# Kernel optimization log

Measured on AMD Instinct MI355X. Metric: run time of the kernel, lower is better.

The kernel has to match this reference:

```python
import jax, jax.numpy as jnp
import numpy as np

B, S, E, D, OUT = 128, 128, 256, 256, 64


def setup_inputs() -> dict:
    key = jax.random.key(0)
    ks = jax.random.split(key, 10)
    w = lambda k, shp, s=0.05: (jax.random.normal(k, shp, dtype=jnp.float32) * s)
    return {
        "input_encoded": jax.random.normal(ks[0], (B, S, E), dtype=jnp.float32),
        "y_history": jax.random.normal(ks[1], (B, S, OUT), dtype=jnp.float32),
        "h0": jax.random.normal(ks[2], (B, D), dtype=jnp.float32) * 0.1,
        "c0": jax.random.normal(ks[3], (B, D), dtype=jnp.float32) * 0.1,
        "attn_W1": w(ks[4], (2 * D + E, E)),
        "attn_b1": jnp.zeros((E,), jnp.float32),
        "attn_w2": w(ks[5], (E,)),
        "attn_b2": jnp.zeros((1,), jnp.float32),
        "lstm_Wih": w(ks[6], (OUT, 4 * D)),
        "lstm_Whh": w(ks[7], (D, 4 * D)),
        "lstm_bih": jnp.zeros((4 * D,), jnp.float32),
        "lstm_bhh": jnp.zeros((4 * D,), jnp.float32),
        "fc_W": w(ks[8], (E + OUT, OUT)),
        "fc_b": jnp.zeros((OUT,), jnp.float32),
        "fc_out_W": w(ks[9], (D + E, OUT * S)),
        "fc_out_b": jnp.zeros((OUT * S,), jnp.float32),
    }


def reference(input_encoded, y_history, h0, c0, attn_W1, attn_b1, attn_w2, attn_b2,
              lstm_Wih, lstm_Whh, lstm_bih, lstm_bhh, fc_W, fc_b, fc_out_W, fc_out_b):
    # Split the attn first-layer weight according to the concat order (h, c, enc).
    Wh, Wc, We = attn_W1[:D], attn_W1[D:2 * D], attn_W1[2 * D:]
    # Encoder projection is time-invariant across decoder steps; hoist it.
    enc_proj = jnp.einsum('bse,ef->bsf', input_encoded, We)  # [B,S,E]

    def step(carry, y_t):
        h, c, _ = carry
        hc = h @ Wh + c @ Wc + attn_b1                       # [B,E]
        pre = jnp.tanh(enc_proj + hc[:, None, :])            # [B,S,E]
        scores = pre @ attn_w2 + attn_b2[0]                  # [B,S]
        alpha = jax.nn.softmax(scores, axis=1)
        context = jnp.einsum('bs,bse->be', alpha, input_encoded)  # [B,E]
        y_tilde = jnp.concatenate([context, y_t], axis=1) @ fc_W + fc_b  # [B,OUT]
        gates = y_tilde @ lstm_Wih + lstm_bih + h @ lstm_Whh + lstm_bhh  # [B,4D]
        i, f, g, o = jnp.split(gates, 4, axis=1)  # pytorch gate order i,f,g,o
        c_new = jax.nn.sigmoid(f) * c + jax.nn.sigmoid(i) * jnp.tanh(g)
        h_new = jax.nn.sigmoid(o) * jnp.tanh(c_new)
        return (h_new, c_new, context), None

    y_seq = jnp.transpose(y_history, (1, 0, 2))  # [S,B,OUT]
    (h_T, c_T, context_T), _ = jax.lax.scan(step, (h0, c0, jnp.zeros((B, E), h0.dtype)), y_seq)
    out = jnp.concatenate([h_T, context_T], axis=1) @ fc_out_W + fc_out_b  # [B,OUT*S]
    return out.reshape(-1, S, OUT)
```

## Files before the change

kernel.cpp:

```cpp
#include <hip/hip_runtime.h>

#define BB 128
#define SS 128
#define EE 256
#define DD 256
#define OO 64

#define W1_OFF   0
#define WHH_OFF  196608
#define WIH_OFF  458752
#define FCW_OFF  524288
#define WTOTAL   544768

__device__ __forceinline__ float fsig(float x) { return 1.0f / (1.0f + __expf(-x)); }
__device__ __forceinline__ float ftanh(float x) {
    float t = __expf(-2.0f * fabsf(x));
    float r = (1.0f - t) / (1.0f + t);
    return copysignf(r, x);
}
__device__ __forceinline__ int SWZ(int e) { return (e & ~31) | ((e + 4 * (e >> 5)) & 31); }

__device__ __forceinline__ void fma8(const uint4 w, const float xv, float* acc) {
    acc[0] += xv * __uint_as_float(w.x << 16);
    acc[1] += xv * __uint_as_float(w.x & 0xffff0000u);
    acc[2] += xv * __uint_as_float(w.y << 16);
    acc[3] += xv * __uint_as_float(w.y & 0xffff0000u);
    acc[4] += xv * __uint_as_float(w.z << 16);
    acc[5] += xv * __uint_as_float(w.z & 0xffff0000u);
    acc[6] += xv * __uint_as_float(w.w << 16);
    acc[7] += xv * __uint_as_float(w.w & 0xffff0000u);
}

__global__ __launch_bounds__(256) void conv_kernel(
    const float* __restrict__ W1, const float* __restrict__ Whh,
    const float* __restrict__ Wih, const float* __restrict__ fcW,
    unsigned short* __restrict__ out)
{
    const int idx = blockIdx.x * 256 + threadIdx.x;
    float f;
    if      (idx < WHH_OFF)  f = W1[idx];
    else if (idx < WIH_OFF)  f = Whh[idx - WHH_OFF];
    else if (idx < FCW_OFF)  f = Wih[idx - WIH_OFF];
    else if (idx < WTOTAL)   f = fcW[idx - FCW_OFF];
    else return;
    unsigned int u = __float_as_uint(f);
    u = (u + 0x7fffu + ((u >> 16) & 1u)) >> 16;
    out[idx] = (unsigned short)u;
}

__global__ __launch_bounds__(1024, 4) void scan_kernel(
    const float* __restrict__ inp,
    const float* __restrict__ yhist,
    const float* __restrict__ h0, const float* __restrict__ c0,
    const float* __restrict__ W1f,
    const float* __restrict__ b1, const float* __restrict__ w2, const float* __restrict__ b2,
    const float* __restrict__ bih, const float* __restrict__ bhh,
    const float* __restrict__ fcb,
    const unsigned short* __restrict__ wbf,
    float* __restrict__ hctxT)
{
    __shared__ float sh_h[DD], sh_c[DD], sh_hc[EE];
    __shared__ float sh_gh[1024];
    __shared__ float sh_w2[EE];
    __shared__ float sh_b1[EE], sh_bs[1024];
    __shared__ float sh_raw[SS];
    __shared__ float sh_ctx[EE], sh_y[OO], sh_yt[OO], sh_fcb[OO];
    __shared__ float sh_misc[1];
    __shared__ float red1[32 * 256];
    __shared__ float red2[8 * 1024];

    const int b = blockIdx.x, t = threadIdx.x;
    const float* inp_b = inp + b * SS * EE;
    const unsigned short* W1bf  = wbf + W1_OFF;
    const unsigned short* Whhbf = wbf + WHH_OFF;
    const unsigned short* Wihbf = wbf + WIH_OFF;
    const unsigned short* fcWbf = wbf + FCW_OFF;
    const float b2v = b2[0];

    const int e8  = (t & 31) * 8,  kc1 = t >> 5;
    const int j8  = (t & 127) * 8, kc2 = t >> 7;
    const int s_own = t >> 3,      a2  = t & 7, e0 = a2 * 32;
    const int e4  = (t & 63) * 4,  sc  = t >> 6;
    const int o4  = (t & 15) * 4,  kc3 = t >> 4;

    if (t < 256) {
        sh_h[t] = h0[b * 256 + t]; sh_c[t] = c0[b * 256 + t];
        sh_b1[t] = b1[t];
        sh_w2[SWZ(t)] = w2[t];
    }
    if (t < 64) sh_fcb[t] = fcb[t];
    sh_bs[t] = bih[t] + bhh[t];

    float er[32];
    #pragma unroll
    for (int j = 0; j < 32; ++j) er[j] = 0.f;
    {
        const float* We = W1f + 512 * 256;
        for (int kc = 0; kc < 16; ++kc) {
            {
                const int row = t >> 6, c4 = (t & 63) * 4;
                float4 v = *(const float4*)(We + (size_t)(kc * 16 + row) * 256 + c4);
                *(float4*)&red1[row * 256 + c4] = v;
            }
            {
                const int s = t >> 3, k2 = (t & 7) * 2;
                float2 v = *(const float2*)(inp_b + s * 256 + kc * 16 + k2);
                red1[4096 + s * 16 + k2] = v.x;
                red1[4096 + s * 16 + k2 + 1] = v.y;
            }
            __syncthreads();
            for (int k = 0; k < 16; ++k) {
                const float xv = red1[4096 + s_own * 16 + k];
                #pragma unroll
                for (int j4 = 0; j4 < 8; ++j4) {
                    float4 w = *(const float4*)&red1[k * 256 + e0 + j4 * 4];
                    er[j4*4+0] += xv * w.x; er[j4*4+1] += xv * w.y;
                    er[j4*4+2] += xv * w.z; er[j4*4+3] += xv * w.w;
                }
            }
            __syncthreads();
        }
    }

    for (int ts = 0; ts < SS; ++ts) {
        if (t < 64) sh_y[t] = yhist[b * SS * OO + ts * OO + t];

        {
            float acc[8];
            #pragma unroll
            for (int r = 0; r < 8; ++r) acc[r] = 0.f;
            #pragma unroll 4
            for (int k = kc1 * 16; k < kc1 * 16 + 16; ++k) {
                const float xv = (k < 256) ? sh_h[k] : sh_c[k - 256];
                uint4 w = *(const uint4*)(W1bf + (size_t)k * 256 + e8);
                fma8(w, xv, acc);
            }
            *(float4*)&red1[kc1 * 256 + e8]     = make_float4(acc[0], acc[1], acc[2], acc[3]);
            *(float4*)&red1[kc1 * 256 + e8 + 4] = make_float4(acc[4], acc[5], acc[6], acc[7]);
        }
        {
            float acc[8];
            #pragma unroll
            for (int r = 0; r < 8; ++r) acc[r] = 0.f;
            #pragma unroll 4
            for (int k = kc2 * 32; k < kc2 * 32 + 32; ++k) {
                const float hv = sh_h[k];
                uint4 w = *(const uint4*)(Whhbf + (size_t)k * 1024 + j8);
                fma8(w, hv, acc);
            }
            *(float4*)&red2[kc2 * 1024 + j8]     = make_float4(acc[0], acc[1], acc[2], acc[3]);
            *(float4*)&red2[kc2 * 1024 + j8 + 4] = make_float4(acc[4], acc[5], acc[6], acc[7]);
        }
        __syncthreads();
        if (t < 256) {
            float v = sh_b1[t];
            #pragma unroll 8
            for (int kc = 0; kc < 32; ++kc) v += red1[kc * 256 + t];
            sh_hc[SWZ(t)] = v;
        }
        {
            float v = 0.f;
            #pragma unroll
            for (int kc = 0; kc < 8; ++kc) v += red2[kc * 1024 + t];
            sh_gh[t] = v;
        }
        __syncthreads();

        {
            float acc = 0.f;
            #pragma unroll
            for (int j4 = 0; j4 < 8; ++j4) {
                const int phys = e0 + ((j4 * 4 + 4 * a2) & 31);
                float4 hc4 = *(const float4*)&sh_hc[phys];
                float4 w24 = *(const float4*)&sh_w2[phys];
                acc += ftanh(er[j4*4+0] + hc4.x) * w24.x;
                acc += ftanh(er[j4*4+1] + hc4.y) * w24.y;
                acc += ftanh(er[j4*4+2] + hc4.z) * w24.z;
                acc += ftanh(er[j4*4+3] + hc4.w) * w24.w;
            }
            acc += __shfl_xor(acc, 1);
            acc += __shfl_xor(acc, 2);
            acc += __shfl_xor(acc, 4);
            if (a2 == 0) sh_raw[s_own] = __expf(acc + b2v);
        }
        __syncthreads();
        if (t < 64) {
            float v = sh_raw[t] + sh_raw[t + 64];
            #pragma unroll
            for (int m = 32; m > 0; m >>= 1) v += __shfl_xor(v, m);
            if (t == 0) sh_misc[0] = 1.0f / v;
        }
        __syncthreads();

        {
            float ax = 0.f, ay = 0.f, az = 0.f, aw = 0.f;
            for (int s = sc * 8; s < sc * 8 + 8; ++s) {
                const float al = sh_raw[s];
                float4 iv = *(const float4*)(inp_b + s * 256 + e4);
                ax += al * iv.x; ay += al * iv.y; az += al * iv.z; aw += al * iv.w;
            }
            *(float4*)&red1[sc * 256 + e4] = make_float4(ax, ay, az, aw);
        }
        __syncthreads();
        if (t < 256) {
            float v = 0.f;
            #pragma unroll
            for (int k = 0; k < 16; ++k) v += red1[k * 256 + t];
            v *= sh_misc[0];
            sh_ctx[t] = v;
            if (ts == SS - 1) hctxT[(size_t)(256 + t) * 128 + b] = v;
        }
        __syncthreads();

        {
            float acc[4] = {0.f, 0.f, 0.f, 0.f};
            for (int kk = kc3 * 5; kk < kc3 * 5 + 5; ++kk) {
                const float val = (kk < 256) ? sh_ctx[kk] : sh_y[kk - 256];
                uint2 w = *(const uint2*)(fcWbf + kk * 64 + o4);
                acc[0] += val * __uint_as_float(w.x << 16);
                acc[1] += val * __uint_as_float(w.x & 0xffff0000u);
                acc[2] += val * __uint_as_float(w.y << 16);
                acc[3] += val * __uint_as_float(w.y & 0xffff0000u);
            }
            *(float4*)&red1[kc3 * 64 + o4] = make_float4(acc[0], acc[1], acc[2], acc[3]);
        }
        __syncthreads();
        if (t < 64) {
            float v = sh_fcb[t];
            #pragma unroll 16
            for (int kc = 0; kc < 64; ++kc) v += red1[kc * 64 + t];
            sh_yt[t] = v;
        }
        __syncthreads();

        {
            float acc[8];
            #pragma unroll
            for (int r = 0; r < 8; ++r) acc[r] = 0.f;
            #pragma unroll
            for (int k = kc2 * 8; k < kc2 * 8 + 8; ++k) {
                const float yv = sh_yt[k];
                uint4 w = *(const uint4*)(Wihbf + (size_t)k * 1024 + j8);
                fma8(w, yv, acc);
            }
            *(float4*)&red2[kc2 * 1024 + j8]     = make_float4(acc[0], acc[1], acc[2], acc[3]);
            *(float4*)&red2[kc2 * 1024 + j8 + 4] = make_float4(acc[4], acc[5], acc[6], acc[7]);
        }
        __syncthreads();
        {
            float v = sh_gh[t] + sh_bs[t];
            #pragma unroll
            for (int kc = 0; kc < 8; ++kc) v += red2[kc * 1024 + t];
            red1[t] = v;
        }
        __syncthreads();
        if (t < 256) {
            const float gi = red1[t], gf = red1[256 + t], gg = red1[512 + t], go = red1[768 + t];
            const float cn = fsig(gf) * sh_c[t] + fsig(gi) * ftanh(gg);
            sh_c[t] = cn;
            const float hn = fsig(go) * ftanh(cn);
            sh_h[t] = hn;
            if (ts == SS - 1) hctxT[(size_t)t * 128 + b] = hn;
        }
        __syncthreads();
    }
}

__global__ __launch_bounds__(256) void out_gemm(
    const float* __restrict__ AT, const float* __restrict__ W,
    const float* __restrict__ bias, float* __restrict__ out)
{
    __shared__ float Ab[64 * 132];
    __shared__ float Bb[64 * 32];
    const int t = threadIdx.x;
    const int nt = blockIdx.x * 32;
    const int n4 = (t & 7) * 4;
    const int m4 = (t >> 3) * 4;
    float acc[4][4];
    #pragma unroll
    for (int i = 0; i < 4; ++i)
        #pragma unroll
        for (int jj = 0; jj < 4; ++jj) acc[i][jj] = 0.f;

    for (int kc = 0; kc < 8; ++kc) {
        #pragma unroll
        for (int i = 0; i < 8; ++i) {
            const int flat4 = i * 256 + t;
            const int row = flat4 >> 5, mm4 = (flat4 & 31) * 4;
            float4 v = *(const float4*)(AT + (size_t)(kc * 64 + row) * 128 + mm4);
            *(float4*)&Ab[row * 132 + mm4] = v;
        }
        #pragma unroll
        for (int i = 0; i < 2; ++i) {
            const int fl = t + i * 256;
            const int k = fl >> 3, nn4 = (fl & 7) * 4;
            *(float4*)&Bb[k * 32 + nn4] =
                *(const float4*)(W + (size_t)(kc * 64 + k) * 8192 + nt + nn4);
        }
        __syncthreads();
        for (int k = 0; k < 64; ++k) {
            const float4 bv = *(const float4*)&Bb[k * 32 + n4];
            const float4 av = *(const float4*)&Ab[k * 132 + m4];
            acc[0][0] += av.x * bv.x; acc[0][1] += av.x * bv.y; acc[0][2] += av.x * bv.z; acc[0][3] += av.x * bv.w;
            acc[1][0] += av.y * bv.x; acc[1][1] += av.y * bv.y; acc[1][2] += av.y * bv.z; acc[1][3] += av.y * bv.w;
            acc[2][0] += av.z * bv.x; acc[2][1] += av.z * bv.y; acc[2][2] += av.z * bv.z; acc[2][3] += av.z * bv.w;
            acc[3][0] += av.w * bv.x; acc[3][1] += av.w * bv.y; acc[3][2] += av.w * bv.z; acc[3][3] += av.w * bv.w;
        }
        __syncthreads();
    }
    const float4 bb = *(const float4*)(bias + nt + n4);
    #pragma unroll
    for (int i = 0; i < 4; ++i) {
        float4 r;
        r.x = acc[i][0] + bb.x; r.y = acc[i][1] + bb.y;
        r.z = acc[i][2] + bb.z; r.w = acc[i][3] + bb.w;
        *(float4*)(out + (size_t)(m4 + i) * 8192 + nt + n4) = r;
    }
}

extern "C" void kernel_launch(void* const* d_in, const int* in_sizes, int n_in,
                              void* d_out, int out_size, void* d_ws, size_t ws_size,
                              hipStream_t stream) {
    const float* inp = (const float*)d_in[0];
    const float* yh  = (const float*)d_in[1];
    const float* h0  = (const float*)d_in[2];
    const float* c0  = (const float*)d_in[3];
    const float* W1  = (const float*)d_in[4];
    const float* b1  = (const float*)d_in[5];
    const float* w2  = (const float*)d_in[6];
    const float* b2  = (const float*)d_in[7];
    const float* Wih = (const float*)d_in[8];
    const float* Whh = (const float*)d_in[9];
    const float* bih = (const float*)d_in[10];
    const float* bhh = (const float*)d_in[11];
    const float* fcW = (const float*)d_in[12];
    const float* fcb = (const float*)d_in[13];
    const float* foW = (const float*)d_in[14];
    const float* fob = (const float*)d_in[15];

    float* hctxT = (float*)d_ws;
    unsigned short* wbf = (unsigned short*)d_out;

    conv_kernel<<<dim3((WTOTAL + 255) / 256), dim3(256), 0, stream>>>(W1, Whh, Wih, fcW, wbf);
    scan_kernel<<<dim3(BB), dim3(1024), 0, stream>>>(
        inp, yh, h0, c0, W1, b1, w2, b2, bih, bhh, fcb, wbf, hctxT);
    out_gemm<<<dim3(8192 / 32), dim3(256), 0, stream>>>(hctxT, foW, fob, (float*)d_out);
}
```

Measured before the change: 4.855 ms.

## Cache encoder input in LDS, prefetch Wih into registers, rebalance matvec splits

Loads the block's whole encoder input slice (128x256 floats, padded) into shared memory once, so the per-step context reduction reads LDS instead of global memory. It prefetches the Wih bf16 weights into registers ahead of the y_tilde dependency, so those global loads overlap the context and fc work. It also regroups the h/c and Whh matvecs into narrower columns with deeper k-chunks, separates the attention hc reduction so it finishes before the Whh matvec, and folds bias b1 into the encoder projection registers. The large shared buffer (about 150KB) raises LDS usage per block and adds register pressure from the prefetch array.

```diff
diff --git a/kernel.cpp b/kernel.cpp
--- a/kernel.cpp
+++ b/kernel.cpp
@@ -19,17 +19,8 @@
     return copysignf(r, x);
 }
 __device__ __forceinline__ int SWZ(int e) { return (e & ~31) | ((e + 4 * (e >> 5)) & 31); }
-
-__device__ __forceinline__ void fma8(const uint4 w, const float xv, float* acc) {
-    acc[0] += xv * __uint_as_float(w.x << 16);
-    acc[1] += xv * __uint_as_float(w.x & 0xffff0000u);
-    acc[2] += xv * __uint_as_float(w.y << 16);
-    acc[3] += xv * __uint_as_float(w.y & 0xffff0000u);
-    acc[4] += xv * __uint_as_float(w.z << 16);
-    acc[5] += xv * __uint_as_float(w.z & 0xffff0000u);
-    acc[6] += xv * __uint_as_float(w.w << 16);
-    acc[7] += xv * __uint_as_float(w.w & 0xffff0000u);
-}
+__device__ __forceinline__ float bflo(unsigned int u) { return __uint_as_float(u << 16); }
+__device__ __forceinline__ float bfhi(unsigned int u) { return __uint_as_float(u & 0xffff0000u); }
 
 __global__ __launch_bounds__(256) void conv_kernel(
     const float* __restrict__ W1, const float* __restrict__ Whh,
@@ -59,37 +50,44 @@
     const unsigned short* __restrict__ wbf,
     float* __restrict__ hctxT)
 {
-    __shared__ float sh_h[DD], sh_c[DD], sh_hc[EE];
-    __shared__ float sh_gh[1024];
+    __shared__ float sh_inp[SS * 260];
+    __shared__ float red[5 * 1024];
+    __shared__ float sh_h[DD], sh_c[DD];
+    __shared__ float sh_hc[EE];
     __shared__ float sh_w2[EE];
-    __shared__ float sh_b1[EE], sh_bs[1024];
     __shared__ float sh_raw[SS];
-    __shared__ float sh_ctx[EE], sh_y[OO], sh_yt[OO], sh_fcb[OO];
+    __shared__ float sh_ctx[EE];
+    __shared__ float sh_y[OO], sh_yt[OO];
     __shared__ float sh_misc[1];
-    __shared__ float red1[32 * 256];
-    __shared__ float red2[8 * 1024];
 
     const int b = blockIdx.x, t = threadIdx.x;
-    const float* inp_b = inp + b * SS * EE;
+    const float* inp_b = inp + (size_t)b * SS * EE;
     const unsigned short* W1bf  = wbf + W1_OFF;
     const unsigned short* Whhbf = wbf + WHH_OFF;
     const unsigned short* Wihbf = wbf + WIH_OFF;
     const unsigned short* fcWbf = wbf + FCW_OFF;
     const float b2v = b2[0];
 
-    const int e8  = (t & 31) * 8,  kc1 = t >> 5;
-    const int j8  = (t & 127) * 8, kc2 = t >> 7;
-    const int s_own = t >> 3,      a2  = t & 7, e0 = a2 * 32;
-    const int e4  = (t & 63) * 4,  sc  = t >> 6;
-    const int o4  = (t & 15) * 4,  kc3 = t >> 4;
-
+    const int c0_1 = (t & 63) * 4,  kg1 = t >> 6;
+    const int c0_2 = (t & 255) * 4, kg2 = t >> 8;
+    const int s_own = t >> 3, a2 = t & 7, e0 = a2 * 32;
+    const int c0_3 = (t & 127) * 2, sg3 = t >> 7;
+    const int o4 = (t & 15) * 4, kc3 = t >> 4;
+
+    const float bs_reg  = bih[t] + bhh[t];
+    const float fcb_reg = (t < 64) ? fcb[t] : 0.f;
+
+    #pragma unroll
+    for (int i = 0; i < 8; ++i) {
+        const int idx = i * 1024 + t;
+        const int s = idx >> 6, c4 = (idx & 63) * 4;
+        *(float4*)&sh_inp[s * 260 + c4] = *(const float4*)(inp_b + (size_t)idx * 4);
+    }
     if (t < 256) {
         sh_h[t] = h0[b * 256 + t]; sh_c[t] = c0[b * 256 + t];
-        sh_b1[t] = b1[t];
         sh_w2[SWZ(t)] = w2[t];
     }
-    if (t < 64) sh_fcb[t] = fcb[t];
-    sh_bs[t] = bih[t] + bhh[t];
+    __syncthreads();
 
     float er[32];
     #pragma unroll
@@ -99,73 +97,65 @@
         for (int kc = 0; kc < 16; ++kc) {
             {
                 const int row = t >> 6, c4 = (t & 63) * 4;
-                float4 v = *(const float4*)(We + (size_t)(kc * 16 + row) * 256 + c4);
-                *(float4*)&red1[row * 256 + c4] = v;
-            }
-            {
-                const int s = t >> 3, k2 = (t & 7) * 2;
-                float2 v = *(const float2*)(inp_b + s * 256 + kc * 16 + k2);
-                red1[4096 + s * 16 + k2] = v.x;
-                red1[4096 + s * 16 + k2 + 1] = v.y;
+                *(float4*)&red[row * 256 + c4] =
+                    *(const float4*)(We + (size_t)(kc * 16 + row) * 256 + c4);
             }
             __syncthreads();
             for (int k = 0; k < 16; ++k) {
-                const float xv = red1[4096 + s_own * 16 + k];
+                const float xv = sh_inp[s_own * 260 + kc * 16 + k];
                 #pragma unroll
                 for (int j4 = 0; j4 < 8; ++j4) {
-                    float4 w = *(const float4*)&red1[k * 256 + e0 + j4 * 4];
+                    float4 w = *(const float4*)&red[k * 256 + e0 + j4 * 4];
                     er[j4*4+0] += xv * w.x; er[j4*4+1] += xv * w.y;
                     er[j4*4+2] += xv * w.z; er[j4*4+3] += xv * w.w;
                 }
             }
             __syncthreads();
         }
+        if (t < 256) red[t] = b1[t];
+        __syncthreads();
+        #pragma unroll
+        for (int j4 = 0; j4 < 8; ++j4) {
+            float4 v = *(const float4*)&red[e0 + j4 * 4];
+            er[j4*4+0] += v.x; er[j4*4+1] += v.y; er[j4*4+2] += v.z; er[j4*4+3] += v.w;
+        }
+        __syncthreads();
     }
 
     for (int ts = 0; ts < SS; ++ts) {
-        if (t < 64) sh_y[t] = yhist[b * SS * OO + ts * OO + t];
-
-        {
-            float acc[8];
-            #pragma unroll
-            for (int r = 0; r < 8; ++r) acc[r] = 0.f;
-            #pragma unroll 4
-            for (int k = kc1 * 16; k < kc1 * 16 + 16; ++k) {
+        if (t < 64) sh_y[t] = yhist[(size_t)b * SS * OO + ts * OO + t];
+
+        {
+            float a0 = 0.f, a1 = 0.f, a2v = 0.f, a3 = 0.f;
+            #pragma unroll 8
+            for (int k = kg1 * 32; k < kg1 * 32 + 32; ++k) {
                 const float xv = (k < 256) ? sh_h[k] : sh_c[k - 256];
-                uint4 w = *(const uint4*)(W1bf + (size_t)k * 256 + e8);
-                fma8(w, xv, acc);
-            }
-            *(float4*)&red1[kc1 * 256 + e8]     = make_float4(acc[0], acc[1], acc[2], acc[3]);
-            *(float4*)&red1[kc1 * 256 + e8 + 4] = make_float4(acc[4], acc[5], acc[6], acc[7]);
-        }
-        {
-            float acc[8];
-            #pragma unroll
-            for (int r = 0; r < 8; ++r) acc[r] = 0.f;
-            #pragma unroll 4
-            for (int k = kc2 * 32; k < kc2 * 32 + 32; ++k) {
+                uint2 w = *(const uint2*)(W1bf + (size_t)k * 256 + c0_1);
+                a0  += xv * bflo(w.x); a1 += xv * bfhi(w.x);
+                a2v += xv * bflo(w.y); a3 += xv * bfhi(w.y);
+            }
+            *(float4*)&red[kg1 * 256 + c0_1] = make_float4(a0, a1, a2v, a3);
+        }
+        __syncthreads();
+        if (t < 256) {
+            float v = 0.f;
+            #pragma unroll
+            for (int kg = 0; kg < 16; ++kg) v += red[kg * 256 + t];
+            sh_hc[SWZ(t)] = v;
+        }
+        __syncthreads();
+
+        {
+            float a0 = 0.f, a1 = 0.f, a2v = 0.f, a3 = 0.f;
+            #pragma unroll 8
+            for (int k = kg2 * 64; k < kg2 * 64 + 64; ++k) {
                 const float hv = sh_h[k];
-                uint4 w = *(const uint4*)(Whhbf + (size_t)k * 1024 + j8);
-                fma8(w, hv, acc);
-            }
-            *(float4*)&red2[kc2 * 1024 + j8]     = make_float4(acc[0], acc[1], acc[2], acc[3]);
-            *(float4*)&red2[kc2 * 1024 + j8 + 4] = make_float4(acc[4], acc[5], acc[6], acc[7]);
-        }
-        __syncthreads();
-        if (t < 256) {
-            float v = sh_b1[t];
-            #pragma unroll 8
-            for (int kc = 0; kc < 32; ++kc) v += red1[kc * 256 + t];
-            sh_hc[SWZ(t)] = v;
-        }
-        {
-            float v = 0.f;
-            #pragma unroll
-            for (int kc = 0; kc < 8; ++kc) v += red2[kc * 1024 + t];
-            sh_gh[t] = v;
-        }
-        __syncthreads();
-
+                uint2 w = *(const uint2*)(Whhbf + (size_t)k * 1024 + c0_2);
+                a0  += hv * bflo(w.x); a1 += hv * bfhi(w.x);
+                a2v += hv * bflo(w.y); a3 += hv * bfhi(w.y);
+            }
+            *(float4*)&red[kg2 * 1024 + c0_2] = make_float4(a0, a1, a2v, a3);
+        }
         {
             float acc = 0.f;
             #pragma unroll
@@ -184,6 +174,14 @@
             if (a2 == 0) sh_raw[s_own] = __expf(acc + b2v);
         }
         __syncthreads();
+
+        float gh_reg;
+        {
+            float v = bs_reg;
+            #pragma unroll
+            for (int kg = 0; kg < 4; ++kg) v += red[kg * 1024 + t];
+            gh_reg = v;
+        }
         if (t < 64) {
             float v = sh_raw[t] + sh_raw[t + 64];
             #pragma unroll
@@ -192,20 +190,26 @@
         }
         __syncthreads();
 
-        {
-            float ax = 0.f, ay = 0.f, az = 0.f, aw = 0.f;
-            for (int s = sc * 8; s < sc * 8 + 8; ++s) {
+        uint2 wpre[16];
+        #pragma unroll
+        for (int i = 0; i < 16; ++i)
+            wpre[i] = *(const uint2*)(Wihbf + (size_t)(kg2 * 16 + i) * 1024 + c0_2);
+        {
+            float ax = 0.f, ay = 0.f;
+            #pragma unroll
+            for (int i = 0; i < 16; ++i) {
+                const int s = sg3 * 16 + i;
                 const float al = sh_raw[s];
-                float4 iv = *(const float4*)(inp_b + s * 256 + e4);
-                ax += al * iv.x; ay += al * iv.y; az += al * iv.z; aw += al * iv.w;
-            }
-            *(float4*)&red1[sc * 256 + e4] = make_float4(ax, ay, az, aw);
+                ax += al * sh_inp[s * 260 + c0_3];
+                ay += al * sh_inp[s * 260 + c0_3 + 1];
+            }
+            *(float2*)&red[sg3 * 256 + c0_3] = make_float2(ax, ay);
         }
         __syncthreads();
         if (t < 256) {
             float v = 0.f;
             #pragma unroll
-            for (int k = 0; k < 16; ++k) v += red1[k * 256 + t];
+            for (int sg = 0; sg < 8; ++sg) v += red[sg * 256 + t];
             v *= sh_misc[0];
             sh_ctx[t] = v;
             if (ts == SS - 1) hctxT[(size_t)(256 + t) * 128 + b] = v;
@@ -213,49 +217,46 @@
         __syncthreads();
 
         {
-            float acc[4] = {0.f, 0.f, 0.f, 0.f};
+            float a0 = 0.f, a1 = 0.f, a2v = 0.f, a3 = 0.f;
             for (int kk = kc3 * 5; kk < kc3 * 5 + 5; ++kk) {
                 const float val = (kk < 256) ? sh_ctx[kk] : sh_y[kk - 256];
                 uint2 w = *(const uint2*)(fcWbf + kk * 64 + o4);
-                acc[0] += val * __uint_as_float(w.x << 16);
-                acc[1] += val * __uint_as_float(w.x & 0xffff0000u);
-                acc[2] += val * __uint_as_float(w.y << 16);
-                acc[3] += val * __uint_as_float(w.y & 0xffff0000u);
-            }
-            *(float4*)&red1[kc3 * 64 + o4] = make_float4(acc[0], acc[1], acc[2], acc[3]);
+                a0  += val * bflo(w.x); a1 += val * bfhi(w.x);
+                a2v += val * bflo(w.y); a3 += val * bfhi(w.y);
+            }
+            *(float4*)&red[kc3 * 64 + o4] = make_float4(a0, a1, a2v, a3);
         }
         __syncthreads();
         if (t < 64) {
-            float v = sh_fcb[t];
+            float v = fcb_reg;
             #pragma unroll 16
-            for (int kc = 0; kc < 64; ++kc) v += red1[kc * 64 + t];
+            for (int kg = 0; kg < 64; ++kg) v += red[kg * 64 + t];
             sh_yt[t] = v;
         }
         __syncthreads();
 
         {
-            float acc[8];
-            #pragma unroll
-            for (int r = 0; r < 8; ++r) acc[r] = 0.f;
-            #pragma unroll
-            for (int k = kc2 * 8; k < kc2 * 8 + 8; ++k) {
-                const float yv = sh_yt[k];
-                uint4 w = *(const uint4*)(Wihbf + (size_t)k * 1024 + j8);
-                fma8(w, yv, acc);
-            }
-            *(float4*)&red2[kc2 * 1024 + j8]     = make_float4(acc[0], acc[1], acc[2], acc[3]);
-            *(float4*)&red2[kc2 * 1024 + j8 + 4] = make_float4(acc[4], acc[5], acc[6], acc[7]);
-        }
-        __syncthreads();
-        {
-            float v = sh_gh[t] + sh_bs[t];
-            #pragma unroll
-            for (int kc = 0; kc < 8; ++kc) v += red2[kc * 1024 + t];
-            red1[t] = v;
+            float a0 = 0.f, a1 = 0.f, a2v = 0.f, a3 = 0.f;
+            #pragma unroll
+            for (int i = 0; i < 16; ++i) {
+                const float yv = sh_yt[kg2 * 16 + i];
+                const uint2 w = wpre[i];
+                a0  += yv * bflo(w.x); a1 += yv * bfhi(w.x);
+                a2v += yv * bflo(w.y); a3 += yv * bfhi(w.y);
+            }
+            *(float4*)&red[kg2 * 1024 + c0_2] = make_float4(a0, a1, a2v, a3);
+        }
+        __syncthreads();
+        {
+            float g = gh_reg;
+            #pragma unroll
+            for (int kg = 0; kg < 4; ++kg) g += red[kg * 1024 + t];
+            red[4096 + t] = g;
         }
         __syncthreads();
         if (t < 256) {
-            const float gi = red1[t], gf = red1[256 + t], gg = red1[512 + t], go = red1[768 + t];
+            const float gi = red[4096 + t], gf = red[4096 + 256 + t];
+            const float gg = red[4096 + 512 + t], go = red[4096 + 768 + t];
             const float cn = fsig(gf) * sh_c[t] + fsig(gi) * ftanh(gg);
             sh_c[t] = cn;
             const float hn = fsig(go) * ftanh(cn);
```

Result: slower. 5.672 ms (+16.8%).

## Prefetch weight and input tiles into registers ahead of use across phases

Applied to the files above, without the earlier changes.

Loads of the bf16 weight slices for the W1, Whh and Wih mat-vecs, the input tile for the context sum, and the next step's y_history value are issued earlier into register arrays. Empty asm pins keep the compiler from sinking the loads, so global-memory latency overlaps preceding compute and barriers. The first half of each thread's W1 slice is reloaded at the end of every step so it is ready for the next one. This raises register pressure and could lower occupancy or cause spills.

```diff
diff --git a/kernel.cpp b/kernel.cpp
--- a/kernel.cpp
+++ b/kernel.cpp
@@ -12,6 +12,9 @@
 #define FCW_OFF  524288
 #define WTOTAL   544768
 
+#define PIN4(v_) asm volatile("" : "+v"((v_).x), "+v"((v_).y), "+v"((v_).z), "+v"((v_).w))
+#define PIN1(v_) asm volatile("" : "+v"(v_))
+
 __device__ __forceinline__ float fsig(float x) { return 1.0f / (1.0f + __expf(-x)); }
 __device__ __forceinline__ float ftanh(float x) {
     float t = __expf(-2.0f * fabsf(x));
@@ -19,16 +22,14 @@
     return copysignf(r, x);
 }
 __device__ __forceinline__ int SWZ(int e) { return (e & ~31) | ((e + 4 * (e >> 5)) & 31); }
+__device__ __forceinline__ float bflo(unsigned int u) { return __uint_as_float(u << 16); }
+__device__ __forceinline__ float bfhi(unsigned int u) { return __uint_as_float(u & 0xffff0000u); }
 
 __device__ __forceinline__ void fma8(const uint4 w, const float xv, float* acc) {
-    acc[0] += xv * __uint_as_float(w.x << 16);
-    acc[1] += xv * __uint_as_float(w.x & 0xffff0000u);
-    acc[2] += xv * __uint_as_float(w.y << 16);
-    acc[3] += xv * __uint_as_float(w.y & 0xffff0000u);
-    acc[4] += xv * __uint_as_float(w.z << 16);
-    acc[5] += xv * __uint_as_float(w.z & 0xffff0000u);
-    acc[6] += xv * __uint_as_float(w.w << 16);
-    acc[7] += xv * __uint_as_float(w.w & 0xffff0000u);
+    acc[0] += xv * bflo(w.x); acc[1] += xv * bfhi(w.x);
+    acc[2] += xv * bflo(w.y); acc[3] += xv * bfhi(w.y);
+    acc[4] += xv * bflo(w.z); acc[5] += xv * bfhi(w.z);
+    acc[6] += xv * bflo(w.w); acc[7] += xv * bfhi(w.w);
 }
 
 __global__ __launch_bounds__(256) void conv_kernel(
@@ -70,7 +71,7 @@
     __shared__ float red2[8 * 1024];
 
     const int b = blockIdx.x, t = threadIdx.x;
-    const float* inp_b = inp + b * SS * EE;
+    const float* inp_b = inp + (size_t)b * SS * EE;
     const unsigned short* W1bf  = wbf + W1_OFF;
     const unsigned short* Whhbf = wbf + WHH_OFF;
     const unsigned short* Wihbf = wbf + WIH_OFF;
@@ -122,19 +123,36 @@
         }
     }
 
+    const unsigned short* W1p1  = W1bf  + (size_t)(kc1 * 16) * 256 + e8;
+    const unsigned short* Whhp  = Whhbf + (size_t)(kc2 * 32) * 1024 + j8;
+    const unsigned short* Wihp  = Wihbf + (size_t)(kc2 * 8) * 1024 + j8;
+
+    uint4 p1w[8];
+    #pragma unroll
+    for (int i = 0; i < 8; ++i) { p1w[i] = *(const uint4*)(W1p1 + i * 256); PIN4(p1w[i]); }
+    float yreg = 0.f;
+    if (t < 64) yreg = yhist[(size_t)b * SS * OO + t];
+
     for (int ts = 0; ts < SS; ++ts) {
-        if (t < 64) sh_y[t] = yhist[b * SS * OO + ts * OO + t];
+        if (t < 64) sh_y[t] = yreg;
 
         {
             float acc[8];
             #pragma unroll
             for (int r = 0; r < 8; ++r) acc[r] = 0.f;
-            #pragma unroll 4
-            for (int k = kc1 * 16; k < kc1 * 16 + 16; ++k) {
-                const float xv = (k < 256) ? sh_h[k] : sh_c[k - 256];
-                uint4 w = *(const uint4*)(W1bf + (size_t)k * 256 + e8);
-                fma8(w, xv, acc);
-            }
+            uint4 wb1[8];
+            #pragma unroll
+            for (int i = 0; i < 8; ++i) wb1[i] = *(const uint4*)(W1p1 + (8 + i) * 256);
+            const float* xsrc = (kc1 < 16) ? &sh_h[kc1 * 16] : &sh_c[kc1 * 16 - 256];
+            float xv[16];
+            #pragma unroll
+            for (int i = 0; i < 16; ++i) xv[i] = xsrc[i];
+            #pragma unroll
+            for (int i = 0; i < 8; ++i) fma8(p1w[i], xv[i], acc);
+            #pragma unroll
+            for (int i = 0; i < 8; ++i) PIN4(wb1[i]);
+            #pragma unroll
+            for (int i = 0; i < 8; ++i) fma8(wb1[i], xv[8 + i], acc);
             *(float4*)&red1[kc1 * 256 + e8]     = make_float4(acc[0], acc[1], acc[2], acc[3]);
             *(float4*)&red1[kc1 * 256 + e8 + 4] = make_float4(acc[4], acc[5], acc[6], acc[7]);
         }
@@ -142,11 +160,19 @@
             float acc[8];
             #pragma unroll
             for (int r = 0; r < 8; ++r) acc[r] = 0.f;
-            #pragma unroll 4
-            for (int k = kc2 * 32; k < kc2 * 32 + 32; ++k) {
-                const float hv = sh_h[k];
-                uint4 w = *(const uint4*)(Whhbf + (size_t)k * 1024 + j8);
-                fma8(w, hv, acc);
+            const float* hsrc = &sh_h[kc2 * 32];
+            #pragma unroll
+            for (int c = 0; c < 4; ++c) {
+                uint4 wb[8];
+                #pragma unroll
+                for (int i = 0; i < 8; ++i) wb[i] = *(const uint4*)(Whhp + (c * 8 + i) * 1024);
+                float hv[8];
+                #pragma unroll
+                for (int i = 0; i < 8; ++i) hv[i] = hsrc[c * 8 + i];
+                #pragma unroll
+                for (int i = 0; i < 8; ++i) PIN4(wb[i]);
+                #pragma unroll
+                for (int i = 0; i < 8; ++i) fma8(wb[i], hv[i], acc);
             }
             *(float4*)&red2[kc2 * 1024 + j8]     = make_float4(acc[0], acc[1], acc[2], acc[3]);
             *(float4*)&red2[kc2 * 1024 + j8 + 4] = make_float4(acc[4], acc[5], acc[6], acc[7]);
@@ -165,6 +191,10 @@
             sh_gh[t] = v;
         }
         __syncthreads();
+
+        uint4 wih[8];
+        #pragma unroll
+        for (int i = 0; i < 8; ++i) wih[i] = *(const uint4*)(Wihp + i * 1024);
 
         {
             float acc = 0.f;
@@ -183,6 +213,8 @@
             acc += __shfl_xor(acc, 4);
             if (a2 == 0) sh_raw[s_own] = __expf(acc + b2v);
         }
+        #pragma unroll
+        for (int i = 0; i < 8; ++i) PIN4(wih[i]);
         __syncthreads();
         if (t < 64) {
             float v = sh_raw[t] + sh_raw[t + 64];
@@ -193,11 +225,25 @@
         __syncthreads();
 
         {
+            float4 iv[8];
+            #pragma unroll
+            for (int i = 0; i < 8; ++i)
+                iv[i] = *(const float4*)(inp_b + (size_t)(sc * 8 + i) * 256 + e4);
+            if (t < 64) {
+                const int tn = (ts + 1) & (SS - 1);
+                yreg = yhist[(size_t)b * SS * OO + tn * OO + t];
+                PIN1(yreg);
+            }
+            float al[8];
+            #pragma unroll
+            for (int i = 0; i < 8; ++i) al[i] = sh_raw[sc * 8 + i];
+            #pragma unroll
+            for (int i = 0; i < 8; ++i) PIN4(iv[i]);
             float ax = 0.f, ay = 0.f, az = 0.f, aw = 0.f;
-            for (int s = sc * 8; s < sc * 8 + 8; ++s) {
-                const float al = sh_raw[s];
-                float4 iv = *(const float4*)(inp_b + s * 256 + e4);
-                ax += al * iv.x; ay += al * iv.y; az += al * iv.z; aw += al * iv.w;
+            #pragma unroll
+            for (int i = 0; i < 8; ++i) {
+                ax += al[i] * iv[i].x; ay += al[i] * iv[i].y;
+                az += al[i] * iv[i].z; aw += al[i] * iv[i].w;
             }
             *(float4*)&red1[sc * 256 + e4] = make_float4(ax, ay, az, aw);
         }
@@ -217,10 +263,10 @@
             for (int kk = kc3 * 5; kk < kc3 * 5 + 5; ++kk) {
                 const float val = (kk < 256) ? sh_ctx[kk] : sh_y[kk - 256];
                 uint2 w = *(const uint2*)(fcWbf + kk * 64 + o4);
-                acc[0] += val * __uint_as_float(w.x << 16);
-                acc[1] += val * __uint_as_float(w.x & 0xffff0000u);
-                acc[2] += val * __uint_as_float(w.y << 16);
-                acc[3] += val * __uint_as_float(w.y & 0xffff0000u);
+                acc[0] += val * bflo(w.x);
+                acc[1] += val * bfhi(w.x);
+                acc[2] += val * bflo(w.y);
+                acc[3] += val * bfhi(w.y);
             }
             *(float4*)&red1[kc3 * 64 + o4] = make_float4(acc[0], acc[1], acc[2], acc[3]);
         }
@@ -234,18 +280,19 @@
         __syncthreads();
 
         {
+            float yv[8];
+            #pragma unroll
+            for (int i = 0; i < 8; ++i) yv[i] = sh_yt[kc2 * 8 + i];
             float acc[8];
             #pragma unroll
             for (int r = 0; r < 8; ++r) acc[r] = 0.f;
             #pragma unroll
-            for (int k = kc2 * 8; k < kc2 * 8 + 8; ++k) {
-                const float yv = sh_yt[k];
-                uint4 w = *(const uint4*)(Wihbf + (size_t)k * 1024 + j8);
-                fma8(w, yv, acc);
-            }
+            for (int i = 0; i < 8; ++i) fma8(wih[i], yv[i], acc);
             *(float4*)&red2[kc2 * 1024 + j8]     = make_float4(acc[0], acc[1], acc[2], acc[3]);
             *(float4*)&red2[kc2 * 1024 + j8 + 4] = make_float4(acc[4], acc[5], acc[6], acc[7]);
         }
+        #pragma unroll
+        for (int i = 0; i < 8; ++i) { p1w[i] = *(const uint4*)(W1p1 + i * 256); PIN4(p1w[i]); }
         __syncthreads();
         {
             float v = sh_gh[t] + sh_bs[t];
```

Measured after the change: 5.419 ms. +11.6%, slower.

## Stream Whh through double-buffered LDS with async global_load_lds prefetch

Applied to the files above, without the earlier changes.

The recurrent Whh matrix-vector product now stages bf16 Whh rows into a two-slot LDS buffer using global_load_lds async copies, prefetching two chunks ahead. The prefetch wraps around so the next timestep's first chunks are already loading. The aim is to hide global/L2 load latency on the serial per-step critical path. In exchange it adds 64KB of LDS, two workgroup barriers per chunk (32 per step), and a manual vmcnt wait that relies on load ordering. Helpers for bf16 unpacking and size_t index casts are cosmetic.

```diff
diff --git a/kernel.cpp b/kernel.cpp
--- a/kernel.cpp
+++ b/kernel.cpp
@@ -19,16 +19,20 @@
     return copysignf(r, x);
 }
 __device__ __forceinline__ int SWZ(int e) { return (e & ~31) | ((e + 4 * (e >> 5)) & 31); }
+__device__ __forceinline__ float bflo(unsigned int u) { return __uint_as_float(u << 16); }
+__device__ __forceinline__ float bfhi(unsigned int u) { return __uint_as_float(u & 0xffff0000u); }
 
 __device__ __forceinline__ void fma8(const uint4 w, const float xv, float* acc) {
-    acc[0] += xv * __uint_as_float(w.x << 16);
-    acc[1] += xv * __uint_as_float(w.x & 0xffff0000u);
-    acc[2] += xv * __uint_as_float(w.y << 16);
-    acc[3] += xv * __uint_as_float(w.y & 0xffff0000u);
-    acc[4] += xv * __uint_as_float(w.z << 16);
-    acc[5] += xv * __uint_as_float(w.z & 0xffff0000u);
-    acc[6] += xv * __uint_as_float(w.w << 16);
-    acc[7] += xv * __uint_as_float(w.w & 0xffff0000u);
+    acc[0] += xv * bflo(w.x); acc[1] += xv * bfhi(w.x);
+    acc[2] += xv * bflo(w.y); acc[3] += xv * bfhi(w.y);
+    acc[4] += xv * bflo(w.z); acc[5] += xv * bfhi(w.z);
+    acc[6] += xv * bflo(w.w); acc[7] += xv * bfhi(w.w);
+}
+
+__device__ __forceinline__ void gld16(const unsigned short* g, unsigned short* l) {
+    __builtin_amdgcn_global_load_lds(
+        (const __attribute__((address_space(1))) unsigned int*)g,
+        (__attribute__((address_space(3))) unsigned int*)l, 16, 0, 0);
 }
 
 __global__ __launch_bounds__(256) void conv_kernel(
@@ -68,9 +72,10 @@
     __shared__ float sh_misc[1];
     __shared__ float red1[32 * 256];
     __shared__ float red2[8 * 1024];
+    __shared__ __align__(16) unsigned short sh_stage[2][16 * 1024];
 
     const int b = blockIdx.x, t = threadIdx.x;
-    const float* inp_b = inp + b * SS * EE;
+    const float* inp_b = inp + (size_t)b * SS * EE;
     const unsigned short* W1bf  = wbf + W1_OFF;
     const unsigned short* Whhbf = wbf + WHH_OFF;
     const unsigned short* Wihbf = wbf + WIH_OFF;
@@ -82,6 +87,7 @@
     const int s_own = t >> 3,      a2  = t & 7, e0 = a2 * 32;
     const int e4  = (t & 63) * 4,  sc  = t >> 6;
     const int o4  = (t & 15) * 4,  kc3 = t >> 4;
+    const int wv  = t >> 6, lane = t & 63;
 
     if (t < 256) {
         sh_h[t] = h0[b * 256 + t]; sh_c[t] = c0[b * 256 + t];
@@ -122,8 +128,17 @@
         }
     }
 
+    {
+        const unsigned short* g0 = Whhbf + (size_t)0 * 16384 + wv * 1024 + lane * 8;
+        gld16(g0,       &sh_stage[0][wv * 1024]);
+        gld16(g0 + 512, &sh_stage[0][wv * 1024 + 512]);
+        const unsigned short* g1 = Whhbf + (size_t)1 * 16384 + wv * 1024 + lane * 8;
+        gld16(g1,       &sh_stage[1][wv * 1024]);
+        gld16(g1 + 512, &sh_stage[1][wv * 1024 + 512]);
+    }
+
     for (int ts = 0; ts < SS; ++ts) {
-        if (t < 64) sh_y[t] = yhist[b * SS * OO + ts * OO + t];
+        if (t < 64) sh_y[t] = yhist[(size_t)b * SS * OO + ts * OO + t];
 
         {
             float acc[8];
@@ -138,15 +153,31 @@
             *(float4*)&red1[kc1 * 256 + e8]     = make_float4(acc[0], acc[1], acc[2], acc[3]);
             *(float4*)&red1[kc1 * 256 + e8 + 4] = make_float4(acc[4], acc[5], acc[6], acc[7]);
         }
+
         {
             float acc[8];
             #pragma unroll
             for (int r = 0; r < 8; ++r) acc[r] = 0.f;
-            #pragma unroll 4
-            for (int k = kc2 * 32; k < kc2 * 32 + 32; ++k) {
-                const float hv = sh_h[k];
-                uint4 w = *(const uint4*)(Whhbf + (size_t)k * 1024 + j8);
-                fma8(w, hv, acc);
+            for (int c = 0; c < 16; ++c) {
+                asm volatile("s_waitcnt vmcnt(2)" ::: "memory");
+                __builtin_amdgcn_sched_barrier(0);
+                __builtin_amdgcn_s_barrier();
+                const unsigned short* ls = &sh_stage[c & 1][0];
+                #pragma unroll
+                for (int r = 0; r < 2; ++r) {
+                    const int row = 2 * kc2 + r;
+                    const float hv = sh_h[16 * c + row];
+                    uint4 w = *(const uint4*)(ls + row * 1024 + j8);
+                    fma8(w, hv, acc);
+                }
+                __builtin_amdgcn_s_barrier();
+                {
+                    const int cn = (c + 2) & 15;
+                    const unsigned short* g = Whhbf + (size_t)cn * 16384 + wv * 1024 + lane * 8;
+                    unsigned short* l = &sh_stage[cn & 1][wv * 1024];
+                    gld16(g, l);
+                    gld16(g + 512, l + 512);
+                }
             }
             *(float4*)&red2[kc2 * 1024 + j8]     = make_float4(acc[0], acc[1], acc[2], acc[3]);
             *(float4*)&red2[kc2 * 1024 + j8 + 4] = make_float4(acc[4], acc[5], acc[6], acc[7]);
@@ -217,10 +248,10 @@
             for (int kk = kc3 * 5; kk < kc3 * 5 + 5; ++kk) {
                 const float val = (kk < 256) ? sh_ctx[kk] : sh_y[kk - 256];
                 uint2 w = *(const uint2*)(fcWbf + kk * 64 + o4);
-                acc[0] += val * __uint_as_float(w.x << 16);
-                acc[1] += val * __uint_as_float(w.x & 0xffff0000u);
-                acc[2] += val * __uint_as_float(w.y << 16);
-                acc[3] += val * __uint_as_float(w.y & 0xffff0000u);
+                acc[0] += val * bflo(w.x);
+                acc[1] += val * bfhi(w.x);
+                acc[2] += val * bflo(w.y);
+                acc[3] += val * bfhi(w.y);
             }
             *(float4*)&red1[kc3 * 64 + o4] = make_float4(acc[0], acc[1], acc[2], acc[3]);
         }
```

Measured after the change: 6.078 ms. 25.2% more time.
